# Optimization experiments

Measured on AMD Instinct MI355X. Metric: run time of the kernel, lower is better.

Reference implementation:

```python
import jax, jax.numpy as jnp
import numpy as np

B, S = 4, 2048          # batch, seq_len
IN, OUT = 4096, 4096    # in_features, out_features
SPARSITY = 0.05         # ortho_ratio: fraction of outlier residual entries
ALPHA = 1.0             # privacy switch (set_privacy) -> residual enabled


def setup_inputs() -> dict:
    key = jax.random.key(0)
    k1, k2, k3, k4, k5 = jax.random.split(key, 5)
    x = jax.random.normal(k1, (B, S, IN), dtype=jnp.float32)
    # packed int4 weights: two (value+8) nibbles per byte, values in [0,15]
    base_packed = jax.random.randint(k2, (OUT, IN // 2), 0, 256, dtype=jnp.int32)
    # per-output-row scales = row_max/7, realistic small magnitudes
    scales = jax.random.uniform(k3, (OUT, 1), dtype=jnp.float32, minval=1e-3, maxval=2e-2)
    mask = jax.random.bernoulli(k4, SPARSITY, (OUT, IN))
    w_ortho = jax.random.normal(k5, (OUT, IN), dtype=jnp.float32) * 0.01 * mask
    return {"x": x, "base_packed": base_packed, "scales": scales, "w_ortho": w_ortho}


def _dequant(base_packed, scales):
    # unpack: even input columns are the low nibble, odd columns the high nibble
    low = base_packed & 0xF
    high = (base_packed >> 4) & 0xF
    offs = jnp.stack([low, high], axis=-1).reshape(base_packed.shape[0], -1)  # [OUT, IN]
    return (offs.astype(jnp.float32) - 8.0) * scales  # int4 value * per-row scale


def reference(x, base_packed, scales, w_ortho):
    # out = x @ (W_base + alpha * W_ortho)^T  (fused dequant-GEMM + CSR residual in the kernel)
    w = _dequant(base_packed, scales) + ALPHA * w_ortho  # [OUT, IN]
    return jnp.einsum('bsi,oi->bso', x, w)  # [B, S, OUT], fp32 like the kernel
```

## Files before the change

### kernel.cpp

```cpp
#include <hip/hip_runtime.h>
#include <stdint.h>


#define M_TOTAL 8192
#define N_TOTAL 4096
#define K_TOTAL 4096

typedef __attribute__((ext_vector_type(8)))  __bf16          bf16x8;
typedef __attribute__((ext_vector_type(4)))  float           floatx4;
typedef __attribute__((ext_vector_type(8)))  unsigned short  ushort8;
typedef __attribute__((ext_vector_type(4)))  float           f32x4;
typedef __attribute__((ext_vector_type(4)))  int             intx4;

__device__ __forceinline__ unsigned short f2bf(float f) {
    union { float f; uint32_t u; } c; c.f = f;
    uint32_t u = c.u + 0x7FFFu + ((c.u >> 16) & 1u);
    return (unsigned short)(u >> 16);
}

#define CVT_BLOCKS 16384
#define DEQ_BLOCKS 8192

__global__ __launch_bounds__(256) void prep_kernel(
    const float* __restrict__ x,
    const int*   __restrict__ packed,
    const float* __restrict__ scales,
    const float* __restrict__ ortho,
    unsigned short* __restrict__ xb,
    unsigned short* __restrict__ wb)
{
    const int blk = blockIdx.x;
    if (blk < CVT_BLOCKS) {
        const size_t t = (size_t)blk * 256 + threadIdx.x;
        const f32x4* xv = (const f32x4*)x;
        f32x4 v0 = xv[2 * t];
        f32x4 v1 = xv[2 * t + 1];
        ushort8 r;
        r[0] = f2bf(v0[0]); r[1] = f2bf(v0[1]); r[2] = f2bf(v0[2]); r[3] = f2bf(v0[3]);
        r[4] = f2bf(v1[0]); r[5] = f2bf(v1[1]); r[6] = f2bf(v1[2]); r[7] = f2bf(v1[3]);
        ((ushort8*)xb)[t] = r;
    } else {
        const int t  = (blk - CVT_BLOCKS) * 256 + threadIdx.x;
        const int o  = t >> 9;
        const int jp = (t & 511) << 2;
        intx4 p = *(const intx4*)(packed + (size_t)o * (K_TOTAL / 2) + jp);
        const float s = scales[o];
        const size_t base = (size_t)o * K_TOTAL + (size_t)jp * 2;
        f32x4 g0 = *(const f32x4*)(ortho + base);
        f32x4 g1 = *(const f32x4*)(ortho + base + 4);
        float g[8] = { g0[0], g0[1], g0[2], g0[3], g1[0], g1[1], g1[2], g1[3] };
        ushort8 r;
#pragma unroll
        for (int i = 0; i < 4; ++i) {
            int pi = p[i];
            float lo = (float)((pi & 0xF) - 8) * s + g[2 * i];
            float hi = (float)(((pi >> 4) & 0xF) - 8) * s + g[2 * i + 1];
            r[2 * i]     = f2bf(lo);
            r[2 * i + 1] = f2bf(hi);
        }
        *(ushort8*)(wb + base) = r;
    }
}

__device__ __forceinline__ void async16(const void* g, void* l) {
    __builtin_amdgcn_global_load_lds(
        (__attribute__((address_space(1))) void*)(g),
        (__attribute__((address_space(3))) void*)(l),
        16, 0, 0);
}

__global__ __launch_bounds__(512, 2) void gemm256_kernel(
    const unsigned short* __restrict__ A,
    const unsigned short* __restrict__ Bm,
    float* __restrict__ C)
{
    __shared__ __attribute__((aligned(16))) unsigned short As[4 * 8192];
    __shared__ __attribute__((aligned(16))) unsigned short Bs[4 * 8192];

    const int tid  = threadIdx.x;
    const int wave = tid >> 6;
    const int lane = tid & 63;
    const int quad = lane >> 4;
    const int r16  = lane & 15;
    const int wm   = wave >> 2;
    const int wn   = wave & 3;

    const int row0 = blockIdx.y * 256;
    const int col0 = blockIdx.x * 256;

    const int sr = tid >> 2;
    const int cs = (tid & 3) ^ ((tid >> 3) & 3);
    const unsigned short* ag0 = A  + (size_t)(row0 + sr) * K_TOTAL + cs * 8;
    const unsigned short* ag1 = ag0 + (size_t)128 * K_TOTAL;
    const unsigned short* bg0 = Bm + (size_t)(col0 + sr) * K_TOTAL + cs * 8;
    const unsigned short* bg1 = bg0 + (size_t)128 * K_TOTAL;

    unsigned short* AsW = As + wave * 512;
    unsigned short* BsW = Bs + wave * 512;

#define STAGE_A(slot, kk) do { \
    async16(ag0 + (kk), AsW + (slot) * 8192); \
    async16(ag1 + (kk), AsW + (slot) * 8192 + 4096); } while (0)
#define STAGE_B(slot, kk) do { \
    async16(bg0 + (kk), BsW + (slot) * 8192); \
    async16(bg1 + (kk), BsW + (slot) * 8192 + 4096); } while (0)

    const int swz   = (r16 >> 1) & 3;
    const int a_ofs = (wm * 128 + r16) * 32 + ((quad ^ swz) << 3);
    const int b_ofs = (wn * 64  + r16) * 32 + ((quad ^ swz) << 3);

#define LDA(slot, m) (*(const bf16x8*)(As + (slot) * 8192 + a_ofs + (m) * 512))
#define LDB(slot, n) (*(const bf16x8*)(Bs + (slot) * 8192 + b_ofs + (n) * 512))

    floatx4 acc[8][4] = {};

#define MROW(mi, ar) \
    acc[mi][0] = __builtin_amdgcn_mfma_f32_16x16x32_bf16(ar, b0, acc[mi][0], 0, 0, 0); \
    acc[mi][1] = __builtin_amdgcn_mfma_f32_16x16x32_bf16(ar, b1, acc[mi][1], 0, 0, 0); \
    acc[mi][2] = __builtin_amdgcn_mfma_f32_16x16x32_bf16(ar, b2, acc[mi][2], 0, 0, 0); \
    acc[mi][3] = __builtin_amdgcn_mfma_f32_16x16x32_bf16(ar, b3, acc[mi][3], 0, 0, 0);

#define SLICE(slot, DOSTAGE, kkst, VMW) do { \
    bf16x8 b0 = LDB(slot, 0), b1 = LDB(slot, 1), b2 = LDB(slot, 2), b3 = LDB(slot, 3); \
    bf16x8 a0 = LDA(slot, 0), a1 = LDA(slot, 1), a2 = LDA(slot, 2), a3 = LDA(slot, 3); \
    bf16x8 a4 = LDA(slot, 4), a5 = LDA(slot, 5), a6 = LDA(slot, 6), a7 = LDA(slot, 7); \
    if (DOSTAGE) { STAGE_A(((slot) + 3) & 3, kkst); STAGE_B(((slot) + 3) & 3, kkst); } \
    __builtin_amdgcn_s_setprio(1); \
    MROW(0, a0) MROW(1, a1) MROW(2, a2) MROW(3, a3) \
    MROW(4, a4) MROW(5, a5) MROW(6, a6) MROW(7, a7) \
    __builtin_amdgcn_s_setprio(0); \
    asm volatile(VMW); \
    __builtin_amdgcn_s_barrier(); \
    __builtin_amdgcn_sched_barrier(0); \
} while (0)

    STAGE_A(0, 0);  STAGE_B(0, 0);
    STAGE_A(1, 32); STAGE_B(1, 32);
    STAGE_A(2, 64); STAGE_B(2, 64);
    STAGE_A(3, 96); STAGE_B(3, 96);
    asm volatile("s_waitcnt vmcnt(12)");
    __builtin_amdgcn_s_barrier();
    __builtin_amdgcn_sched_barrier(0);

    SLICE(0, 0, 0,      "s_waitcnt vmcnt(8)");
    SLICE(1, 1, 4 * 32, "s_waitcnt vmcnt(8)");
    SLICE(2, 1, 5 * 32, "s_waitcnt vmcnt(8)");
    SLICE(3, 1, 6 * 32, "s_waitcnt vmcnt(8)");

#pragma unroll 1
    for (int s4 = 4; s4 <= 120; s4 += 4) {
        const int kkb = (s4 + 3) * 32;
        SLICE(0, 1, kkb,      "s_waitcnt vmcnt(8)");
        SLICE(1, 1, kkb + 32, "s_waitcnt vmcnt(8)");
        SLICE(2, 1, kkb + 64, "s_waitcnt vmcnt(8)");
        SLICE(3, 1, kkb + 96, "s_waitcnt vmcnt(8)");
    }

    SLICE(0, 1, 127 * 32, "s_waitcnt vmcnt(8)");
    SLICE(1, 0, 0,        "s_waitcnt vmcnt(4)");
    SLICE(2, 0, 0,        "s_waitcnt vmcnt(0)");
    SLICE(3, 0, 0,        "s_nop 0");

#undef SLICE
#undef MROW
#undef LDA
#undef LDB
#undef STAGE_A
#undef STAGE_B

#pragma unroll
    for (int mi = 0; mi < 8; ++mi) {
#pragma unroll
        for (int ni = 0; ni < 4; ++ni) {
            const int r = row0 + wm * 128 + mi * 16 + quad * 4;
            const int c = col0 + wn * 64 + ni * 16 + r16;
#pragma unroll
            for (int i = 0; i < 4; ++i)
                C[(size_t)(r + i) * N_TOTAL + c] = acc[mi][ni][i];
        }
    }
}

extern "C" void kernel_launch(void* const* d_in, const int* in_sizes, int n_in,
                              void* d_out, int out_size, void* d_ws, size_t ws_size,
                              hipStream_t stream) {
    const float* x      = (const float*)d_in[0];
    const int*   packed = (const int*)d_in[1];
    const float* scales = (const float*)d_in[2];
    const float* ortho  = (const float*)d_in[3];
    float*       out    = (float*)d_out;

    unsigned short* Xb = (unsigned short*)d_ws;
    unsigned short* Wb = (unsigned short*)((char*)d_ws + (size_t)M_TOTAL * K_TOTAL * 2);

    prep_kernel<<<CVT_BLOCKS + DEQ_BLOCKS, 256, 0, stream>>>(x, packed, scales, ortho, Xb, Wb);

    dim3 grid(N_TOTAL / 256, M_TOTAL / 256);
    gemm256_kernel<<<grid, 512, 0, stream>>>(Xb, Wb, out);
}
```

Measured before the change: 537.8 us.

## Software-pipeline LDS fragment loads one K-slice ahead with register double buffering

Restructures the GEMM main loop so each tile step prefetches the next slice's B fragments and first half of A fragments into alternating even/odd register sets while the MFMAs consume the current set. The prologue now stages three slices instead of four, and the vmcnt waits are adjusted to match. The goal is to hide LDS read latency behind MFMA work. In exchange it needs more VGPRs, which with launch bounds 512,2 could cause spills. It also relies on the new slot and waitcnt bookkeeping being correct.

Measured after the change: 551.2 us. +2.5%, slower.

```diff
diff --git a/kernel.cpp b/kernel.cpp
--- a/kernel.cpp
+++ b/kernel.cpp
@@ -114,21 +114,29 @@
 
     floatx4 acc[8][4] = {};
 
-#define MROW(mi, ar) \
-    acc[mi][0] = __builtin_amdgcn_mfma_f32_16x16x32_bf16(ar, b0, acc[mi][0], 0, 0, 0); \
-    acc[mi][1] = __builtin_amdgcn_mfma_f32_16x16x32_bf16(ar, b1, acc[mi][1], 0, 0, 0); \
-    acc[mi][2] = __builtin_amdgcn_mfma_f32_16x16x32_bf16(ar, b2, acc[mi][2], 0, 0, 0); \
-    acc[mi][3] = __builtin_amdgcn_mfma_f32_16x16x32_bf16(ar, b3, acc[mi][3], 0, 0, 0);
-
-#define SLICE(slot, DOSTAGE, kkst, VMW) do { \
-    bf16x8 b0 = LDB(slot, 0), b1 = LDB(slot, 1), b2 = LDB(slot, 2), b3 = LDB(slot, 3); \
-    bf16x8 a0 = LDA(slot, 0), a1 = LDA(slot, 1), a2 = LDA(slot, 2), a3 = LDA(slot, 3); \
-    bf16x8 a4 = LDA(slot, 4), a5 = LDA(slot, 5), a6 = LDA(slot, 6), a7 = LDA(slot, 7); \
-    if (DOSTAGE) { STAGE_A(((slot) + 3) & 3, kkst); STAGE_B(((slot) + 3) & 3, kkst); } \
+    bf16x8 bE0, bE1, bE2, bE3, aE0, aE1, aE2, aE3;
+    bf16x8 bO0, bO1, bO2, bO3, aO0, aO1, aO2, aO3;
+
+#define MROW(mi, areg, S) \
+    acc[mi][0] = __builtin_amdgcn_mfma_f32_16x16x32_bf16(areg, b##S##0, acc[mi][0], 0, 0, 0); \
+    acc[mi][1] = __builtin_amdgcn_mfma_f32_16x16x32_bf16(areg, b##S##1, acc[mi][1], 0, 0, 0); \
+    acc[mi][2] = __builtin_amdgcn_mfma_f32_16x16x32_bf16(areg, b##S##2, acc[mi][2], 0, 0, 0); \
+    acc[mi][3] = __builtin_amdgcn_mfma_f32_16x16x32_bf16(areg, b##S##3, acc[mi][3], 0, 0, 0);
+
+#define TILE(CS, RS, SS, CUR, NXT, DOSTG, kkst, VMW) do { \
+    bf16x8 x4 = LDA(CS, 4), x5 = LDA(CS, 5), x6 = LDA(CS, 6), x7 = LDA(CS, 7); \
+    b##NXT##0 = LDB(RS, 0); b##NXT##1 = LDB(RS, 1); \
+    b##NXT##2 = LDB(RS, 2); b##NXT##3 = LDB(RS, 3); \
+    a##NXT##0 = LDA(RS, 0); a##NXT##1 = LDA(RS, 1); \
+    a##NXT##2 = LDA(RS, 2); a##NXT##3 = LDA(RS, 3); \
+    if (DOSTG) { STAGE_A(SS, kkst); STAGE_B(SS, kkst); } \
+    __builtin_amdgcn_sched_barrier(0); \
     __builtin_amdgcn_s_setprio(1); \
-    MROW(0, a0) MROW(1, a1) MROW(2, a2) MROW(3, a3) \
-    MROW(4, a4) MROW(5, a5) MROW(6, a6) MROW(7, a7) \
+    MROW(0, a##CUR##0, CUR) MROW(1, a##CUR##1, CUR) \
+    MROW(2, a##CUR##2, CUR) MROW(3, a##CUR##3, CUR) \
+    MROW(4, x4, CUR) MROW(5, x5, CUR) MROW(6, x6, CUR) MROW(7, x7, CUR) \
     __builtin_amdgcn_s_setprio(0); \
+    __builtin_amdgcn_sched_barrier(0); \
     asm volatile(VMW); \
     __builtin_amdgcn_s_barrier(); \
     __builtin_amdgcn_sched_barrier(0); \
@@ -137,31 +145,33 @@
     STAGE_A(0, 0);  STAGE_B(0, 0);
     STAGE_A(1, 32); STAGE_B(1, 32);
     STAGE_A(2, 64); STAGE_B(2, 64);
-    STAGE_A(3, 96); STAGE_B(3, 96);
-    asm volatile("s_waitcnt vmcnt(12)");
+    asm volatile("s_waitcnt vmcnt(4)");
     __builtin_amdgcn_s_barrier();
     __builtin_amdgcn_sched_barrier(0);
-
-    SLICE(0, 0, 0,      "s_waitcnt vmcnt(8)");
-    SLICE(1, 1, 4 * 32, "s_waitcnt vmcnt(8)");
-    SLICE(2, 1, 5 * 32, "s_waitcnt vmcnt(8)");
-    SLICE(3, 1, 6 * 32, "s_waitcnt vmcnt(8)");
+    bE0 = LDB(0, 0); bE1 = LDB(0, 1); bE2 = LDB(0, 2); bE3 = LDB(0, 3);
+    aE0 = LDA(0, 0); aE1 = LDA(0, 1); aE2 = LDA(0, 2); aE3 = LDA(0, 3);
 
 #pragma unroll 1
-    for (int s4 = 4; s4 <= 120; s4 += 4) {
+    for (int s4 = 0; s4 < 124; s4 += 4) {
         const int kkb = (s4 + 3) * 32;
-        SLICE(0, 1, kkb,      "s_waitcnt vmcnt(8)");
-        SLICE(1, 1, kkb + 32, "s_waitcnt vmcnt(8)");
-        SLICE(2, 1, kkb + 64, "s_waitcnt vmcnt(8)");
-        SLICE(3, 1, kkb + 96, "s_waitcnt vmcnt(8)");
-    }
-
-    SLICE(0, 1, 127 * 32, "s_waitcnt vmcnt(8)");
-    SLICE(1, 0, 0,        "s_waitcnt vmcnt(4)");
-    SLICE(2, 0, 0,        "s_waitcnt vmcnt(0)");
-    SLICE(3, 0, 0,        "s_nop 0");
-
-#undef SLICE
+        TILE(0, 1, 3, E, O, 1, kkb,       "s_waitcnt vmcnt(4)");
+        TILE(1, 2, 0, O, E, 1, kkb + 32,  "s_waitcnt vmcnt(4)");
+        TILE(2, 3, 1, E, O, 1, kkb + 64,  "s_waitcnt vmcnt(4)");
+        TILE(3, 0, 2, O, E, 1, kkb + 96,  "s_waitcnt vmcnt(4)");
+    }
+
+    TILE(0, 1, 3, E, O, 1, 127 * 32, "s_waitcnt vmcnt(4)");
+    TILE(1, 2, 0, O, E, 0, 0,        "s_waitcnt vmcnt(0)");
+    TILE(2, 3, 0, E, O, 0, 0,        "s_nop 0");
+    {
+        bf16x8 x4 = LDA(3, 4), x5 = LDA(3, 5), x6 = LDA(3, 6), x7 = LDA(3, 7);
+        __builtin_amdgcn_s_setprio(1);
+        MROW(0, aO0, O) MROW(1, aO1, O) MROW(2, aO2, O) MROW(3, aO3, O)
+        MROW(4, x4, O) MROW(5, x5, O) MROW(6, x6, O) MROW(7, x7, O)
+        __builtin_amdgcn_s_setprio(0);
+    }
+
+#undef TILE
 #undef MROW
 #undef LDA
 #undef LDB
```
